# Performance work log

Hardware: AMD Instinct MI355X
Metric: run time of the kernel (lower is better)

## Reference

```python
import jax, jax.numpy as jnp
import numpy as np

THRESH1 = 0.8      # snn.Leaky threshold
THRESH2 = 1.0      # snn.Synaptic default threshold
FS_SLOPE = 25.0    # surrogate.fast_sigmoid default slope
ATAN_ALPHA = 2.0   # surrogate.atan default alpha
TIME_STEPS = 20

# --- surrogate-gradient spike fns (forward = Heaviside) ---
@jax.custom_vjp
def spike_fs(x):
    return (x > 0).astype(x.dtype)
def _fs_fwd(x):
    return (x > 0).astype(x.dtype), x
def _fs_bwd(res, g):
    return (g / (FS_SLOPE * jnp.abs(res) + 1.0) ** 2,)
spike_fs.defvjp(_fs_fwd, _fs_bwd)

@jax.custom_vjp
def spike_atan(x):
    return (x > 0).astype(x.dtype)
def _at_fwd(x):
    return (x > 0).astype(x.dtype), x
def _at_bwd(res, g):
    return (g * (ATAN_ALPHA / 2.0) / (1.0 + (jnp.pi / 2.0 * ATAN_ALPHA * res) ** 2),)
spike_atan.defvjp(_at_fwd, _at_bwd)


def setup_inputs() -> dict:
    key = jax.random.key(0)
    ks = jax.random.split(key, 4)
    V, E, H, B, S = 32000, 256, 512, 8, 16
    x = jax.random.randint(ks[0], (B, S), 0, V)
    embed = jax.random.normal(ks[1], (V, E), jnp.float32)
    W1 = jax.random.normal(ks[2], (H, E), jnp.float32) / jnp.sqrt(jnp.float32(E))
    b1 = jnp.zeros((H,), jnp.float32)
    W2 = jax.random.normal(ks[3], (V, H), jnp.float32) / jnp.sqrt(jnp.float32(H))
    b2 = jnp.zeros((V,), jnp.float32)
    return dict(x=x, embed=embed, W1=W1, b1=b1, W2=W2, b2=b2,
                beta1=jnp.float32(0.85), alpha2=jnp.float32(0.9), beta2=jnp.float32(0.8))


def _forward(x, embed, W1, b1, W2, b2, beta1, alpha2, beta2):
    B, S = x.shape
    V, H = W2.shape
    b1c = jnp.clip(beta1, 0.0, 1.0)   # snntorch clamps learnable decays
    a2c = jnp.clip(alpha2, 0.0, 1.0)
    b2c = jnp.clip(beta2, 0.0, 1.0)
    # cur1 = fc1(embed(x[:, t])) is constant within the inner time loop
    cur1_all = jnp.einsum('bse,he->bsh', embed[x], W1) + b1  # (B, S, H)

    def seq_step(carry, cur1_t):              # cur1_t: (B, H)
        mem1, syn2, mem2 = carry

        def time_step(c, _):
            mem1, syn2, mem2, _ = c
            # Leaky: reset (subtract) from PREVIOUS mem, detached
            reset1 = jax.lax.stop_gradient((mem1 - THRESH1 > 0).astype(mem1.dtype))
            mem1 = b1c * mem1 + cur1_t - reset1 * THRESH1
            spk1 = spike_fs(mem1 - THRESH1)
            cur2 = spk1 @ W2.T + b2            # (B, V)
            # Synaptic: syn = a*syn + cur; mem = b*mem + syn - reset*thr
            reset2 = jax.lax.stop_gradient((mem2 - THRESH2 > 0).astype(mem2.dtype))
            syn2 = a2c * syn2 + cur2
            mem2 = b2c * mem2 + syn2 - reset2 * THRESH2
            spk2 = spike_atan(mem2 - THRESH2)
            return (mem1, syn2, mem2, spk2), None

        spk2_init = jnp.zeros_like(mem2)
        (mem1, syn2, mem2, spk2), _ = jax.lax.scan(
            time_step, (mem1, syn2, mem2, spk2_init), None, length=TIME_STEPS)
        return (mem1, syn2, mem2), spk2       # only last inner spk2 is emitted

    mem1 = jnp.zeros((B, H), jnp.float32)
    syn2 = jnp.zeros((B, V), jnp.float32)
    mem2 = jnp.zeros((B, V), jnp.float32)
    (mem1, syn2, mem2), outs = jax.lax.scan(
        seq_step, (mem1, syn2, mem2), jnp.swapaxes(cur1_all, 0, 1))
    return jnp.swapaxes(outs, 0, 1), mem1, syn2, mem2   # (B, S, V), states


def reference(x, embed, W1, b1, W2, b2, beta1, alpha2, beta2):
    return _forward(x, embed, W1, b1, W2, b2, beta1, alpha2, beta2)
```

## Files before the change

kernel.cpp:

```cpp
#include <hip/hip_runtime.h>
#include <cstdint>

constexpr int NV = 32000;
constexpr int NE = 256;
constexpr int NH = 512;
constexpr int NB = 8;
constexpr int NS = 16;
constexpr int NT = 20;
constexpr float TH1 = 0.8f;
constexpr float TH2 = 1.0f;

typedef _Float16 f16x8 __attribute__((ext_vector_type(8)));
typedef float f32x4 __attribute__((ext_vector_type(4)));

__device__ inline float clip01(float v) { return fminf(fmaxf(v, 0.f), 1.f); }

#define GL_LDS(gp, lp) \
  __builtin_amdgcn_global_load_lds((const __attribute__((address_space(1))) void*)(gp), \
                                   (__attribute__((address_space(3))) void*)(lp), 16, 0, 0)

__device__ inline void barsched() {
  __builtin_amdgcn_s_barrier();
  __builtin_amdgcn_sched_barrier(0);
}

__global__ void k_cur1(const int* __restrict__ x, const float* __restrict__ embed,
                       const float* __restrict__ W1, const float* __restrict__ b1,
                       float* __restrict__ cur1) {
  __shared__ float e[NE];
  int bs = blockIdx.x;
  int row = x[bs];
  e[threadIdx.x] = embed[(size_t)row * NE + threadIdx.x];
  __syncthreads();
  for (int hh = 0; hh < 2; ++hh) {
    int h = threadIdx.x + hh * 256;
    const float* w = W1 + (size_t)h * NE;
    float acc = 0.f;
#pragma unroll 8
    for (int k = 0; k < NE; ++k) acc = fmaf(e[k], w[k], acc);
    cur1[(size_t)bs * NH + h] = acc + b1[h];
  }
}

__global__ void k_spk1(const float* __restrict__ cur1, const float* __restrict__ pbeta1,
                       _Float16* __restrict__ A2P, float* __restrict__ mem1_out) {
  int g = blockIdx.x * blockDim.x + threadIdx.x;
  int b = g >> 9, h = g & 511;
  float bc = clip01(pbeta1[0]);
  float mem = 0.f;
  const _Float16 one  = (_Float16)1.0f;
  const _Float16 zero = (_Float16)0.0f;
  const int ks  = h >> 6;
  const int col = (h & 63) ^ (b << 3);
  for (int s = 0; s < NS; ++s) {
    float c = cur1[((size_t)b * NS + s) * NH + h];
    for (int t = 0; t < NT; ++t) {
      float rst = (mem > TH1) ? TH1 : 0.f;
      mem = __fsub_rn(__fadd_rn(__fmul_rn(bc, mem), c), rst);
      bool spk = mem > TH1;
      int gs = s * NT + t;
      size_t addr = ((size_t)((gs >> 3) * 8 + ks)) * 4096 + ((gs & 7) * 8 + b) * 64 + col;
      A2P[addr] = spk ? one : zero;
    }
  }
  mem1_out[g] = mem;
}

__global__ __launch_bounds__(1024, 4) void k_fused(
    const _Float16* __restrict__ A2P,
    const float* __restrict__ W2,
    const float* __restrict__ b2,
    const float* __restrict__ pa2, const float* __restrict__ pb2,
    float* __restrict__ out) {
  __shared__ __attribute__((aligned(16))) _Float16 As[2 * 16384];
  __shared__ __attribute__((aligned(16))) float    Cl[2][64 * 132];

  const int tid  = threadIdx.x;
  const int lane = tid & 63;
  const int wid  = tid >> 6;
  const int kh   = wid >> 3;
  const int wm   = (wid >> 2) & 1;
  const int wn   = wid & 3;
  const int n0   = blockIdx.x * 128;

  const int lr  = lane & 15;
  const int lk8 = (lane >> 4) * 8;
  const int sw  = (lr & 7) * 8;
  const int cr  = (lane >> 4) * 4, cc = lane & 15;

  f16x8 bfr[2][8];
#pragma unroll
  for (int ni = 0; ni < 2; ++ni) {
    const int n = n0 + wn * 32 + ni * 16 + lr;
    const float* wp = W2 + (size_t)n * NH;
#pragma unroll
    for (int p = 0; p < 4; ++p) {
#pragma unroll
      for (int kf = 0; kf < 2; ++kf) {
        const int k0 = (2 * p + kh) * 64 + kf * 32 + lk8;
        const float4 wa = *(const float4*)(wp + k0);
        const float4 wb = *(const float4*)(wp + k0 + 4);
        f16x8 v;
        v[0] = (_Float16)wa.x; v[1] = (_Float16)wa.y;
        v[2] = (_Float16)wa.z; v[3] = (_Float16)wa.w;
        v[4] = (_Float16)wb.x; v[5] = (_Float16)wb.y;
        v[6] = (_Float16)wb.z; v[7] = (_Float16)wb.w;
        bfr[ni][p * 2 + kf] = v;
      }
    }
  }

  const float a2  = clip01(pa2[0]);
  const float bcl = clip01(pb2[0]);
  const int vv = tid & 127;
  const int bb = tid >> 7;
  const float b2v = b2[n0 + vv];
  float syn = 0.f, mem = 0.f;
  unsigned spkmask = 0;
  f32x4 acc[2][2] = {};

  const _Float16* pA = A2P + wid * 1024 + lane * 8;
  _Float16* dA = As + wid * 1024;
  auto stage = [&](int g) {
    const _Float16* s = pA + (size_t)g * 16384;
    _Float16* d = dA + (g & 1) * 16384;
    GL_LDS(s, d);
    GL_LDS(s + 512, d + 512);
  };

  asm volatile("s_waitcnt vmcnt(0)" ::: "memory");
  barsched();
  stage(0);
  stage(1);

#define STEP(H, PP, KF)                                                          \
  {                                                                              \
    const int tb  = slot * 16384 + (kh + (PP) * 2) * 4096;                       \
    const int col = ((KF) * 32 + lk8) ^ sw;                                      \
    const f16x8 a0 = *(const f16x8*)&As[tb + (wm * 32 + lr) * 64 + col];         \
    const f16x8 a1 = *(const f16x8*)&As[tb + (wm * 32 + 16 + lr) * 64 + col];    \
    acc[0][0] = __builtin_amdgcn_mfma_f32_16x16x32_f16(a0, bfr[0][(2*(H)+(PP))*2+(KF)], acc[0][0], 0, 0, 0); \
    acc[1][0] = __builtin_amdgcn_mfma_f32_16x16x32_f16(a1, bfr[0][(2*(H)+(PP))*2+(KF)], acc[1][0], 0, 0, 0); \
    acc[0][1] = __builtin_amdgcn_mfma_f32_16x16x32_f16(a0, bfr[1][(2*(H)+(PP))*2+(KF)], acc[0][1], 0, 0, 0); \
    acc[1][1] = __builtin_amdgcn_mfma_f32_16x16x32_f16(a1, bfr[1][(2*(H)+(PP))*2+(KF)], acc[1][1], 0, 0, 0); \
  }

#define PHASE(H)                                                                 \
  {                                                                              \
    const int g = mt * 2 + (H);                                                  \
    const int slot = g & 1;                                                      \
    asm volatile("s_waitcnt vmcnt(0)" ::: "memory");                             \
    barsched();                                                                  \
    if (g < 79) stage(g + 1);                                                    \
    STEP(H, 0, 0) STEP(H, 0, 1) STEP(H, 1, 0) STEP(H, 1, 1)                      \
  }

  for (int mt = 0; mt < 40; ++mt) {
    PHASE(0)
    PHASE(1)
#pragma unroll
    for (int mi = 0; mi < 2; ++mi)
#pragma unroll
      for (int ni = 0; ni < 2; ++ni) {
#pragma unroll
        for (int j = 0; j < 4; ++j)
          Cl[kh][(wm * 32 + mi * 16 + cr + j) * 132 + wn * 32 + ni * 16 + cc] = acc[mi][ni][j];
        acc[mi][ni] = (f32x4){0.f, 0.f, 0.f, 0.f};
      }
    barsched();
#pragma unroll
    for (int st = 0; st < 8; ++st) {
      const int gs = mt * 8 + st;
      const int idx = (st * 8 + bb) * 132 + vv;
      float cur2 = __fadd_rn(__fadd_rn(Cl[0][idx], Cl[1][idx]), b2v);
      float rst = (mem > TH2) ? 1.f : 0.f;
      syn = __fadd_rn(__fmul_rn(a2, syn), cur2);
      mem = __fsub_rn(__fadd_rn(__fmul_rn(bcl, mem), syn), rst);
      if (gs % 20 == 19)
        spkmask |= (mem > TH2 ? 1u : 0u) << (gs / 20);
    }
  }
#undef PHASE
#undef STEP

#pragma unroll
  for (int s = 0; s < NS; ++s)
    out[((size_t)bb * NS + s) * NV + n0 + vv] = (spkmask >> s) & 1 ? 1.f : 0.f;
  out[(size_t)4100096 + (size_t)bb * NV + n0 + vv] = syn;
  out[(size_t)4356096 + (size_t)bb * NV + n0 + vv] = mem;
}

extern "C" void kernel_launch(void* const* d_in, const int* in_sizes, int n_in,
                              void* d_out, int out_size, void* d_ws, size_t ws_size,
                              hipStream_t stream) {
  const int*   x     = (const int*)d_in[0];
  const float* embed = (const float*)d_in[1];
  const float* W1    = (const float*)d_in[2];
  const float* b1    = (const float*)d_in[3];
  const float* W2    = (const float*)d_in[4];
  const float* b2    = (const float*)d_in[5];
  const float* pb1   = (const float*)d_in[6];
  const float* pa2   = (const float*)d_in[7];
  const float* pb2   = (const float*)d_in[8];
  float* out = (float*)d_out;

  char* ws = (char*)d_ws;
  float* cur1 = (float*)ws;
  _Float16* A2P = (_Float16*)(ws + 262144);

  hipLaunchKernelGGL(k_cur1, dim3(NB * NS), dim3(256), 0, stream, x, embed, W1, b1, cur1);
  hipLaunchKernelGGL(k_spk1, dim3(16), dim3(256), 0, stream, cur1, pb1, A2P, out + 4096000);
  hipLaunchKernelGGL(k_fused, dim3(NV / 128), dim3(1024), 0, stream,
                     A2P, W2, b2, pa2, pb2, out);
}
```

Before: 145.2 us.

## Stage full 64-row A tile per iteration and reuse A buffer for cross-K reduction

```diff
diff --git a/kernel.cpp b/kernel.cpp
--- a/kernel.cpp
+++ b/kernel.cpp
@@ -72,8 +72,7 @@
     const float* __restrict__ b2,
     const float* __restrict__ pa2, const float* __restrict__ pb2,
     float* __restrict__ out) {
-  __shared__ __attribute__((aligned(16))) _Float16 As[2 * 16384];
-  __shared__ __attribute__((aligned(16))) float    Cl[2][64 * 132];
+  __shared__ __attribute__((aligned(16))) _Float16 As[2 * 32768];
 
   const int tid  = threadIdx.x;
   const int lane = tid & 63;
@@ -97,7 +96,7 @@
     for (int p = 0; p < 4; ++p) {
 #pragma unroll
       for (int kf = 0; kf < 2; ++kf) {
-        const int k0 = (2 * p + kh) * 64 + kf * 32 + lk8;
+        const int k0 = (kh * 4 + p) * 64 + kf * 32 + lk8;
         const float4 wa = *(const float4*)(wp + k0);
         const float4 wb = *(const float4*)(wp + k0 + 4);
         f16x8 v;
@@ -119,60 +118,67 @@
   unsigned spkmask = 0;
   f32x4 acc[2][2] = {};
 
-  const _Float16* pA = A2P + wid * 1024 + lane * 8;
-  _Float16* dA = As + wid * 1024;
+  const _Float16* pA = A2P + wid * 512 + lane * 8;
+  _Float16* dA = As + wid * 512;
   auto stage = [&](int g) {
-    const _Float16* s = pA + (size_t)g * 16384;
-    _Float16* d = dA + (g & 1) * 16384;
-    GL_LDS(s, d);
-    GL_LDS(s + 512, d + 512);
+    const _Float16* s = pA + (size_t)g * 32768;
+    _Float16* d = dA + (g & 1) * 32768;
+    GL_LDS(s,         d);
+    GL_LDS(s + 8192,  d + 8192);
+    GL_LDS(s + 16384, d + 16384);
+    GL_LDS(s + 24576, d + 24576);
   };
 
   asm volatile("s_waitcnt vmcnt(0)" ::: "memory");
   barsched();
   stage(0);
-  stage(1);
-
-#define STEP(H, PP, KF)                                                          \
+
+#define CHUNK(C)                                                                 \
   {                                                                              \
-    const int tb  = slot * 16384 + (kh + (PP) * 2) * 4096;                       \
-    const int col = ((KF) * 32 + lk8) ^ sw;                                      \
-    const f16x8 a0 = *(const f16x8*)&As[tb + (wm * 32 + lr) * 64 + col];         \
-    const f16x8 a1 = *(const f16x8*)&As[tb + (wm * 32 + 16 + lr) * 64 + col];    \
-    acc[0][0] = __builtin_amdgcn_mfma_f32_16x16x32_f16(a0, bfr[0][(2*(H)+(PP))*2+(KF)], acc[0][0], 0, 0, 0); \
-    acc[1][0] = __builtin_amdgcn_mfma_f32_16x16x32_f16(a1, bfr[0][(2*(H)+(PP))*2+(KF)], acc[1][0], 0, 0, 0); \
-    acc[0][1] = __builtin_amdgcn_mfma_f32_16x16x32_f16(a0, bfr[1][(2*(H)+(PP))*2+(KF)], acc[0][1], 0, 0, 0); \
-    acc[1][1] = __builtin_amdgcn_mfma_f32_16x16x32_f16(a1, bfr[1][(2*(H)+(PP))*2+(KF)], acc[1][1], 0, 0, 0); \
-  }
-
-#define PHASE(H)                                                                 \
-  {                                                                              \
-    const int g = mt * 2 + (H);                                                  \
-    const int slot = g & 1;                                                      \
-    asm volatile("s_waitcnt vmcnt(0)" ::: "memory");                             \
-    barsched();                                                                  \
-    if (g < 79) stage(g + 1);                                                    \
-    STEP(H, 0, 0) STEP(H, 0, 1) STEP(H, 1, 0) STEP(H, 1, 1)                      \
+    const int tb = sb + (kh * 4 + (C)) * 4096;                                   \
+    {                                                                            \
+      const int col = lk8 ^ sw;                                                  \
+      const f16x8 a0 = *(const f16x8*)&As[tb + (wm * 32 + lr) * 64 + col];       \
+      const f16x8 a1 = *(const f16x8*)&As[tb + (wm * 32 + 16 + lr) * 64 + col];  \
+      acc[0][0] = __builtin_amdgcn_mfma_f32_16x16x32_f16(a0, bfr[0][(C)*2], acc[0][0], 0, 0, 0); \
+      acc[1][0] = __builtin_amdgcn_mfma_f32_16x16x32_f16(a1, bfr[0][(C)*2], acc[1][0], 0, 0, 0); \
+      acc[0][1] = __builtin_amdgcn_mfma_f32_16x16x32_f16(a0, bfr[1][(C)*2], acc[0][1], 0, 0, 0); \
+      acc[1][1] = __builtin_amdgcn_mfma_f32_16x16x32_f16(a1, bfr[1][(C)*2], acc[1][1], 0, 0, 0); \
+    }                                                                            \
+    {                                                                            \
+      const int col = (32 + lk8) ^ sw;                                           \
+      const f16x8 a0 = *(const f16x8*)&As[tb + (wm * 32 + lr) * 64 + col];       \
+      const f16x8 a1 = *(const f16x8*)&As[tb + (wm * 32 + 16 + lr) * 64 + col];  \
+      acc[0][0] = __builtin_amdgcn_mfma_f32_16x16x32_f16(a0, bfr[0][(C)*2+1], acc[0][0], 0, 0, 0); \
+      acc[1][0] = __builtin_amdgcn_mfma_f32_16x16x32_f16(a1, bfr[0][(C)*2+1], acc[1][0], 0, 0, 0); \
+      acc[0][1] = __builtin_amdgcn_mfma_f32_16x16x32_f16(a0, bfr[1][(C)*2+1], acc[0][1], 0, 0, 0); \
+      acc[1][1] = __builtin_amdgcn_mfma_f32_16x16x32_f16(a1, bfr[1][(C)*2+1], acc[1][1], 0, 0, 0); \
+    }                                                                            \
   }
 
   for (int mt = 0; mt < 40; ++mt) {
-    PHASE(0)
-    PHASE(1)
+    asm volatile("s_waitcnt vmcnt(0)" ::: "memory");
+    barsched();
+    if (mt < 39) stage(mt + 1);
+    const int sb = (mt & 1) * 32768;
+    CHUNK(0) CHUNK(1) CHUNK(2) CHUNK(3)
+    barsched();
+    float* Cl = (float*)&As[sb];
 #pragma unroll
     for (int mi = 0; mi < 2; ++mi)
 #pragma unroll
       for (int ni = 0; ni < 2; ++ni) {
 #pragma unroll
         for (int j = 0; j < 4; ++j)
-          Cl[kh][(wm * 32 + mi * 16 + cr + j) * 132 + wn * 32 + ni * 16 + cc] = acc[mi][ni][j];
+          Cl[((wm * 32 + mi * 16 + cr + j) * 128 + wn * 32 + ni * 16 + cc) * 2 + kh] = acc[mi][ni][j];
         acc[mi][ni] = (f32x4){0.f, 0.f, 0.f, 0.f};
       }
     barsched();
 #pragma unroll
     for (int st = 0; st < 8; ++st) {
       const int gs = mt * 8 + st;
-      const int idx = (st * 8 + bb) * 132 + vv;
-      float cur2 = __fadd_rn(__fadd_rn(Cl[0][idx], Cl[1][idx]), b2v);
+      const float2 c2 = *(const float2*)&Cl[((st * 8 + bb) * 128 + vv) * 2];
+      float cur2 = __fadd_rn(__fadd_rn(c2.x, c2.y), b2v);
       float rst = (mem > TH2) ? 1.f : 0.f;
       syn = __fadd_rn(__fmul_rn(a2, syn), cur2);
       mem = __fsub_rn(__fadd_rn(__fmul_rn(bcl, mem), syn), rst);
@@ -180,8 +186,7 @@
         spkmask |= (mem > TH2 ? 1u : 0u) << (gs / 20);
     }
   }
-#undef PHASE
-#undef STEP
+#undef CHUNK
 
 #pragma unroll
   for (int s = 0; s < NS; ++s)
```

New measurement: 143.3 us. No clear change (-1.3%).

## Load spike A-fragments directly from global in MFMA layout, drop LDS staging

Applied to the files above, without the earlier changes.

```diff
diff --git a/kernel.cpp b/kernel.cpp
--- a/kernel.cpp
+++ b/kernel.cpp
@@ -15,11 +15,8 @@
 
 __device__ inline float clip01(float v) { return fminf(fmaxf(v, 0.f), 1.f); }
 
-#define GL_LDS(gp, lp) \
-  __builtin_amdgcn_global_load_lds((const __attribute__((address_space(1))) void*)(gp), \
-                                   (__attribute__((address_space(3))) void*)(lp), 16, 0, 0)
-
-__device__ inline void barsched() {
+__device__ inline void bar_lds() {
+  asm volatile("s_waitcnt lgkmcnt(0)" ::: "memory");
   __builtin_amdgcn_s_barrier();
   __builtin_amdgcn_sched_barrier(0);
 }
@@ -43,15 +40,16 @@
 }
 
 __global__ void k_spk1(const float* __restrict__ cur1, const float* __restrict__ pbeta1,
-                       _Float16* __restrict__ A2P, float* __restrict__ mem1_out) {
+                       _Float16* __restrict__ A2F, float* __restrict__ mem1_out) {
   int g = blockIdx.x * blockDim.x + threadIdx.x;
   int b = g >> 9, h = g & 511;
   float bc = clip01(pbeta1[0]);
   float mem = 0.f;
   const _Float16 one  = (_Float16)1.0f;
   const _Float16 zero = (_Float16)0.0f;
-  const int ks  = h >> 6;
-  const int col = (h & 63) ^ (b << 3);
+  const int kfi = h >> 5;
+  const int lhi = (h & 31) >> 3;
+  const int e   = h & 7;
   for (int s = 0; s < NS; ++s) {
     float c = cur1[((size_t)b * NS + s) * NH + h];
     for (int t = 0; t < NT; ++t) {
@@ -59,21 +57,22 @@
       mem = __fsub_rn(__fadd_rn(__fmul_rn(bc, mem), c), rst);
       bool spk = mem > TH1;
       int gs = s * NT + t;
-      size_t addr = ((size_t)((gs >> 3) * 8 + ks)) * 4096 + ((gs & 7) * 8 + b) * 64 + col;
-      A2P[addr] = spk ? one : zero;
+      int row = (gs & 7) * 8 + b;
+      int lane = lhi * 16 + (row & 15);
+      size_t addr = ((((size_t)(gs >> 3) * 16 + kfi) * 4 + (row >> 4)) * 64 + lane) * 8 + e;
+      A2F[addr] = spk ? one : zero;
     }
   }
   mem1_out[g] = mem;
 }
 
 __global__ __launch_bounds__(1024, 4) void k_fused(
-    const _Float16* __restrict__ A2P,
+    const _Float16* __restrict__ A2F,
     const float* __restrict__ W2,
     const float* __restrict__ b2,
     const float* __restrict__ pa2, const float* __restrict__ pb2,
     float* __restrict__ out) {
-  __shared__ __attribute__((aligned(16))) _Float16 As[2 * 16384];
-  __shared__ __attribute__((aligned(16))) float    Cl[2][64 * 132];
+  __shared__ float Cl[2][64 * 132];
 
   const int tid  = threadIdx.x;
   const int lane = tid & 63;
@@ -85,7 +84,6 @@
 
   const int lr  = lane & 15;
   const int lk8 = (lane >> 4) * 8;
-  const int sw  = (lr & 7) * 8;
   const int cr  = (lane >> 4) * 4, cc = lane & 15;
 
   f16x8 bfr[2][8];
@@ -97,7 +95,7 @@
     for (int p = 0; p < 4; ++p) {
 #pragma unroll
       for (int kf = 0; kf < 2; ++kf) {
-        const int k0 = (2 * p + kh) * 64 + kf * 32 + lk8;
+        const int k0 = (kh * 4 + p) * 64 + kf * 32 + lk8;
         const float4 wa = *(const float4*)(wp + k0);
         const float4 wb = *(const float4*)(wp + k0 + 4);
         f16x8 v;
@@ -119,45 +117,40 @@
   unsigned spkmask = 0;
   f32x4 acc[2][2] = {};
 
-  const _Float16* pA = A2P + wid * 1024 + lane * 8;
-  _Float16* dA = As + wid * 1024;
-  auto stage = [&](int g) {
-    const _Float16* s = pA + (size_t)g * 16384;
-    _Float16* d = dA + (g & 1) * 16384;
-    GL_LDS(s, d);
-    GL_LDS(s + 512, d + 512);
-  };
-
-  asm volatile("s_waitcnt vmcnt(0)" ::: "memory");
-  barsched();
-  stage(0);
-  stage(1);
-
-#define STEP(H, PP, KF)                                                          \
-  {                                                                              \
-    const int tb  = slot * 16384 + (kh + (PP) * 2) * 4096;                       \
-    const int col = ((KF) * 32 + lk8) ^ sw;                                      \
-    const f16x8 a0 = *(const f16x8*)&As[tb + (wm * 32 + lr) * 64 + col];         \
-    const f16x8 a1 = *(const f16x8*)&As[tb + (wm * 32 + 16 + lr) * 64 + col];    \
-    acc[0][0] = __builtin_amdgcn_mfma_f32_16x16x32_f16(a0, bfr[0][(2*(H)+(PP))*2+(KF)], acc[0][0], 0, 0, 0); \
-    acc[1][0] = __builtin_amdgcn_mfma_f32_16x16x32_f16(a1, bfr[0][(2*(H)+(PP))*2+(KF)], acc[1][0], 0, 0, 0); \
-    acc[0][1] = __builtin_amdgcn_mfma_f32_16x16x32_f16(a0, bfr[1][(2*(H)+(PP))*2+(KF)], acc[0][1], 0, 0, 0); \
-    acc[1][1] = __builtin_amdgcn_mfma_f32_16x16x32_f16(a1, bfr[1][(2*(H)+(PP))*2+(KF)], acc[1][1], 0, 0, 0); \
-  }
-
-#define PHASE(H)                                                                 \
-  {                                                                              \
-    const int g = mt * 2 + (H);                                                  \
-    const int slot = g & 1;                                                      \
-    asm volatile("s_waitcnt vmcnt(0)" ::: "memory");                             \
-    barsched();                                                                  \
-    if (g < 79) stage(g + 1);                                                    \
-    STEP(H, 0, 0) STEP(H, 0, 1) STEP(H, 1, 0) STEP(H, 1, 1)                      \
-  }
+  const _Float16* pAW = A2F + (size_t)kh * 16384 + wm * 1024 + lane * 8;
+
+  f16x8 x0, x1, x2, x3, y0, y1, y2, y3;
+
+#define LOADC(MT, P, S0, S1, S2, S3)                                          \
+  {                                                                           \
+    const _Float16* fb = pAW + (size_t)(MT) * 32768 + (P) * 4096;             \
+    S0 = *(const f16x8*)(fb);                                    \
+    S1 = *(const f16x8*)(fb + 512);                              \
+    S2 = *(const f16x8*)(fb + 2048);                             \
+    S3 = *(const f16x8*)(fb + 2560);                             \
+  }
+
+#define MFMAC(P, S0, S1, S2, S3)                                              \
+  {                                                                           \
+    acc[0][0] = __builtin_amdgcn_mfma_f32_16x16x32_f16(S0, bfr[0][(P)*2], acc[0][0], 0, 0, 0); \
+    acc[1][0] = __builtin_amdgcn_mfma_f32_16x16x32_f16(S1, bfr[0][(P)*2], acc[1][0], 0, 0, 0); \
+    acc[0][1] = __builtin_amdgcn_mfma_f32_16x16x32_f16(S0, bfr[1][(P)*2], acc[0][1], 0, 0, 0); \
+    acc[1][1] = __builtin_amdgcn_mfma_f32_16x16x32_f16(S1, bfr[1][(P)*2], acc[1][1], 0, 0, 0); \
+    acc[0][0] = __builtin_amdgcn_mfma_f32_16x16x32_f16(S2, bfr[0][(P)*2+1], acc[0][0], 0, 0, 0); \
+    acc[1][0] = __builtin_amdgcn_mfma_f32_16x16x32_f16(S3, bfr[0][(P)*2+1], acc[1][0], 0, 0, 0); \
+    acc[0][1] = __builtin_amdgcn_mfma_f32_16x16x32_f16(S2, bfr[1][(P)*2+1], acc[0][1], 0, 0, 0); \
+    acc[1][1] = __builtin_amdgcn_mfma_f32_16x16x32_f16(S3, bfr[1][(P)*2+1], acc[1][1], 0, 0, 0); \
+  }
+
+  LOADC(0, 0, x0, x1, x2, x3);
 
   for (int mt = 0; mt < 40; ++mt) {
-    PHASE(0)
-    PHASE(1)
+    LOADC(mt, 1, y0, y1, y2, y3);  MFMAC(0, x0, x1, x2, x3);
+    LOADC(mt, 2, x0, x1, x2, x3);  MFMAC(1, y0, y1, y2, y3);
+    LOADC(mt, 3, y0, y1, y2, y3);  MFMAC(2, x0, x1, x2, x3);
+    if (mt < 39) LOADC(mt + 1, 0, x0, x1, x2, x3);
+    MFMAC(3, y0, y1, y2, y3);
+
 #pragma unroll
     for (int mi = 0; mi < 2; ++mi)
 #pragma unroll
@@ -167,7 +160,7 @@
           Cl[kh][(wm * 32 + mi * 16 + cr + j) * 132 + wn * 32 + ni * 16 + cc] = acc[mi][ni][j];
         acc[mi][ni] = (f32x4){0.f, 0.f, 0.f, 0.f};
       }
-    barsched();
+    bar_lds();
 #pragma unroll
     for (int st = 0; st < 8; ++st) {
       const int gs = mt * 8 + st;
@@ -179,9 +172,10 @@
       if (gs % 20 == 19)
         spkmask |= (mem > TH2 ? 1u : 0u) << (gs / 20);
     }
-  }
-#undef PHASE
-#undef STEP
+    bar_lds();
+  }
+#undef LOADC
+#undef MFMAC
 
 #pragma unroll
   for (int s = 0; s < NS; ++s)
@@ -206,10 +200,10 @@
 
   char* ws = (char*)d_ws;
   float* cur1 = (float*)ws;
-  _Float16* A2P = (_Float16*)(ws + 262144);
+  _Float16* A2F = (_Float16*)(ws + 262144);
 
   hipLaunchKernelGGL(k_cur1, dim3(NB * NS), dim3(256), 0, stream, x, embed, W1, b1, cur1);
-  hipLaunchKernelGGL(k_spk1, dim3(16), dim3(256), 0, stream, cur1, pb1, A2P, out + 4096000);
+  hipLaunchKernelGGL(k_spk1, dim3(16), dim3(256), 0, stream, cur1, pb1, A2F, out + 4096000);
   hipLaunchKernelGGL(k_fused, dim3(NV / 128), dim3(1024), 0, stream,
-                     A2P, W2, b2, pa2, pb2, out);
-}
+                     A2F, W2, b2, pa2, pb2, out);
+}
```

Measured after the change: 170.6 us. 17.5% more time.
